# Kernel optimization log

Hardware: AMD Instinct MI355X
Metric: run time of the kernel (lower is better)

## Reference

```python
import jax, jax.numpy as jnp
import numpy as np

B, L, D, H = 2, 8192, 1024, 16
HD = D // H  # head_dim = 64


def setup_inputs() -> dict:
    key = jax.random.key(0)
    ks = jax.random.split(key, 5)
    s = 1.0 / np.sqrt(D)
    return {
        "x": jax.random.normal(ks[0], (B, L, D), dtype=jnp.float32),
        "Wq": jax.random.normal(ks[1], (D, D), dtype=jnp.float32) * s,
        "bq": jnp.zeros((D,), dtype=jnp.float32),
        "Wk": jax.random.normal(ks[2], (D, D), dtype=jnp.float32) * s,
        "bk": jnp.zeros((D,), dtype=jnp.float32),
        "Wv": jax.random.normal(ks[3], (D, D), dtype=jnp.float32) * s,
        "bv": jnp.zeros((D,), dtype=jnp.float32),
        "Wo": jax.random.normal(ks[4], (D, D), dtype=jnp.float32) * s,
        "bo": jnp.zeros((D,), dtype=jnp.float32),
    }


def _rotary(seq_len, dim):
    pos = jnp.arange(seq_len, dtype=jnp.float32)
    freq = 1.0 / (10000.0 ** (jnp.arange(0, dim, 2, dtype=jnp.float32) / dim))
    ang = pos[:, None] * freq[None, :]               # (L, dim/2)
    sin, cos = jnp.sin(ang), jnp.cos(ang)
    # interleave-duplicate: stack((s,s),-1).reshape(L,dim)  (matches torch code)
    sin = jnp.stack((sin, sin), axis=-1).reshape(seq_len, dim)
    cos = jnp.stack((cos, cos), axis=-1).reshape(seq_len, dim)
    return sin, cos


def _rotate_half(t):
    t1, t2 = jnp.split(t, 2, axis=-1)
    return jnp.concatenate([-t2, t1], axis=-1)


def reference(x, Wq, bq, Wk, bk, Wv, bv, Wo, bo):
    b, l, d = x.shape
    q = (x @ Wq + bq).reshape(b, l, H, HD)
    k = (x @ Wk + bk).reshape(b, l, H, HD)
    v = (x @ Wv + bv).reshape(b, l, H, HD)

    sin, cos = _rotary(l, HD)
    sin = sin[None, :, None, :]  # (1, L, 1, HD)
    cos = cos[None, :, None, :]
    q = q * cos + _rotate_half(q) * sin
    k = k * cos + _rotate_half(k) * sin

    # NOTE: faithful to original — heads NOT transposed to (B,H,L,HD),
    # so scores are (B, L, H, H): attention mixes across heads per position.
    scores = jnp.einsum('blhd,bled->blhe', q, k) / jnp.sqrt(jnp.float32(HD))
    w = jax.nn.softmax(scores, axis=-1)              # dropout = identity (eval)
    out = jnp.einsum('blhe,bled->blhd', w, v).reshape(b, l, d)
    return out @ Wo + bo
```

## Files before the change

kernel.cpp:

```cpp
#include <hip/hip_runtime.h>
#include <hip/hip_bf16.h>

typedef __bf16 bf16_t;
typedef __bf16 bf16x8 __attribute__((ext_vector_type(8)));
typedef float f32x4 __attribute__((ext_vector_type(4)));

#define SEQ_L 8192
#define DMODEL 1024
#define NHEAD 16
#define HDIM 64
static constexpr int MROWS = 2 * SEQ_L;

__device__ __forceinline__ void async_cp16(const bf16_t* g, bf16_t* l) {
  __builtin_amdgcn_global_load_lds(
      (__attribute__((address_space(1))) void*)(void*)(g),
      (__attribute__((address_space(3))) void*)(void*)(l), 16, 0, 0);
}
__device__ __forceinline__ void wg_barrier() { __builtin_amdgcn_s_barrier(); }

__global__ __launch_bounds__(256) void f32_to_bf16_k(const float* __restrict__ in,
                                                     bf16_t* __restrict__ out, int n) {
  int i = (blockIdx.x * 256 + threadIdx.x) * 8;
  if (i >= n) return;
  float4 a = *(const float4*)(in + i);
  float4 b = *(const float4*)(in + i + 4);
  bf16x8 o;
  o[0] = (__bf16)a.x; o[1] = (__bf16)a.y; o[2] = (__bf16)a.z; o[3] = (__bf16)a.w;
  o[4] = (__bf16)b.x; o[5] = (__bf16)b.y; o[6] = (__bf16)b.z; o[7] = (__bf16)b.w;
  *(bf16x8*)(out + i) = o;
}

__global__ __launch_bounds__(256) void w_to_bt_k(
    const float* __restrict__ W0, const float* __restrict__ W1,
    const float* __restrict__ W2, const float* __restrict__ W3,
    bf16_t* __restrict__ T0, bf16_t* __restrict__ T1,
    bf16_t* __restrict__ T2, bf16_t* __restrict__ T3) {
  __shared__ float tile[32][33];
  const int z = blockIdx.z;
  const float* W = (z == 0) ? W0 : (z == 1) ? W1 : (z == 2) ? W2 : W3;
  bf16_t* T = (z == 0) ? T0 : (z == 1) ? T1 : (z == 2) ? T2 : T3;
  const int bx = blockIdx.x, by = blockIdx.y;
  const int tx = threadIdx.x, ty = threadIdx.y;
#pragma unroll
  for (int r = 0; r < 4; ++r)
    tile[ty + r * 8][tx] = W[(size_t)(by * 32 + ty + r * 8) * DMODEL + bx * 32 + tx];
  __syncthreads();
#pragma unroll
  for (int r = 0; r < 4; ++r)
    T[(size_t)(bx * 32 + ty + r * 8) * DMODEL + by * 32 + tx] = (bf16_t)tile[tx][ty + r * 8];
}

__global__ __launch_bounds__(256) void rope_tab_k(float2* __restrict__ tab) {
  int i = blockIdx.x * 256 + threadIdx.x;
  int pos = i >> 5, j = i & 31;
  double freq = pow(10000.0, -(double)j / 32.0);
  double ang = (double)pos * freq;
  tab[i] = make_float2((float)cos(ang), (float)sin(ang));
}

template <int MODE>
__global__ __launch_bounds__(256, 4) void gemm128(
    const bf16_t* __restrict__ A, const bf16_t* __restrict__ Bt,
    const float* __restrict__ b0, const float* __restrict__ b1,
    const float* __restrict__ b2, const float2* __restrict__ rope,
    void* __restrict__ O0, void* __restrict__ O1, void* __restrict__ O2) {
  constexpr int K = DMODEL;
  constexpr int KT = K / 64;
  __shared__ bf16_t As_[128 * 64];
  __shared__ bf16_t Bs_[128 * 64];
  const int tid = threadIdx.x;
  const int lane = tid & 63;
  const int wave = tid >> 6;
  const int wm = wave >> 1;
  const int wn = wave & 1;
  const size_t row0 = (size_t)blockIdx.x * 128;
  const int col0 = blockIdx.y * 128;
  const int fr = lane & 15;
  const int fkb = (lane >> 4) * 16;

  const int srow = lane >> 3;
  const int schunk = (lane & 7) ^ (lane >> 3);
  const bf16_t* gA = A + (row0 + wave * 32 + srow) * K + schunk * 8;
  const bf16_t* gB = Bt + ((size_t)col0 + wave * 32 + srow) * K + schunk * 8;
  bf16_t* lA = As_ + wave * 2048 + lane * 8;
  bf16_t* lB = Bs_ + wave * 2048 + lane * 8;

#define STAGE(j)                                           \
  do {                                                     \
    async_cp16(gA + (j)*64, lA);                           \
    async_cp16(gA + 8 * K + (j)*64, lA + 512);             \
    async_cp16(gA + 16 * K + (j)*64, lA + 1024);           \
    async_cp16(gA + 24 * K + (j)*64, lA + 1536);           \
    async_cp16(gB + (j)*64, lB);                           \
    async_cp16(gB + 8 * K + (j)*64, lB + 512);             \
    async_cp16(gB + 16 * K + (j)*64, lB + 1024);           \
    async_cp16(gB + 24 * K + (j)*64, lB + 1536);           \
  } while (0)
#define RD(base, row, kh)                                                    \
  (*(const bf16x8*)((const char*)(base) +                                    \
                    ((((row)*128) + ((kh)*64 + fkb)) ^ (((row)&7) << 4))))
#define VMCNT(n) asm volatile("s_waitcnt vmcnt(" #n ")")
#define LGKM0() asm volatile("s_waitcnt lgkmcnt(0)")
#define SCHED_FENCE() __builtin_amdgcn_sched_barrier(0)

  f32x4 acc[4][4] = {};
  bf16x8 a4[4], b4[4];

  STAGE(0);
  VMCNT(0);
  wg_barrier();
  SCHED_FENCE();

  for (int m = 0; m < KT; ++m) {
#pragma unroll
    for (int f = 0; f < 4; ++f) a4[f] = RD(As_, wm * 64 + f * 16 + fr, 0);
#pragma unroll
    for (int n = 0; n < 4; ++n) b4[n] = RD(Bs_, wn * 64 + n * 16 + fr, 0);
    __builtin_amdgcn_s_setprio(1);
#pragma unroll
    for (int f = 0; f < 4; ++f)
#pragma unroll
      for (int n = 0; n < 4; ++n)
        acc[f][n] = __builtin_amdgcn_mfma_f32_16x16x32_bf16(a4[f], b4[n], acc[f][n], 0, 0, 0);
    __builtin_amdgcn_s_setprio(0);
#pragma unroll
    for (int f = 0; f < 4; ++f) a4[f] = RD(As_, wm * 64 + f * 16 + fr, 1);
#pragma unroll
    for (int n = 0; n < 4; ++n) b4[n] = RD(Bs_, wn * 64 + n * 16 + fr, 1);
    __builtin_amdgcn_s_setprio(1);
#pragma unroll
    for (int f = 0; f < 4; ++f)
#pragma unroll
      for (int n = 0; n < 4; ++n)
        acc[f][n] = __builtin_amdgcn_mfma_f32_16x16x32_bf16(a4[f], b4[n], acc[f][n], 0, 0, 0);
    __builtin_amdgcn_s_setprio(0);
    LGKM0();
    SCHED_FENCE();
    wg_barrier();
    SCHED_FENCE();
    if (m + 1 < KT) STAGE(m + 1);
    VMCNT(0);
    wg_barrier();
    SCHED_FENCE();
  }
#undef STAGE
#undef RD
#undef VMCNT
#undef LGKM0
#undef SCHED_FENCE

  const int lr = (lane >> 4) * 4;
  const int lc = lane & 15;
  const int gcol = col0 + wn * 64;
  int which = 0;
  const float* bias = b0;
  int ocol = gcol;
  if constexpr (MODE == 0) {
    which = gcol >> 10;
    bias = (which == 0) ? b0 : (which == 1) ? b1 : b2;
    ocol = gcol - (which << 10);
  }
  const bool do_rope = (MODE == 0) && (which < 2);
  bf16_t* Cb = nullptr;
  float* Cf = nullptr;
  if constexpr (MODE == 0)
    Cb = (bf16_t*)((which == 0) ? O0 : (which == 1) ? O1 : O2);
  else
    Cf = (float*)O0;

#pragma unroll
  for (int mf = 0; mf < 4; ++mf) {
#pragma unroll
    for (int i = 0; i < 4; ++i) {
      const size_t grow = row0 + wm * 64 + mf * 16 + lr + i;
      float vv[4];
#pragma unroll
      for (int n = 0; n < 4; ++n) vv[n] = acc[mf][n][i] + bias[ocol + n * 16 + lc];
      if (do_rope) {
        const int pos = (int)(grow & (size_t)(SEQ_L - 1));
        const float2* rp = rope + (size_t)pos * 32 + (lc >> 1);
        float rv[4];
#pragma unroll
        for (int n = 0; n < 4; ++n) {
          float2 cs = rp[n * 8];
          rv[n] = (n < 2) ? vv[n] * cs.x - vv[n + 2] * cs.y
                          : vv[n] * cs.x + vv[n - 2] * cs.y;
        }
#pragma unroll
        for (int n = 0; n < 4; ++n) vv[n] = rv[n];
      }
      const size_t cbase = grow * (size_t)DMODEL + ocol + lc;
      if constexpr (MODE == 1) {
#pragma unroll
        for (int n = 0; n < 4; ++n) Cf[cbase + n * 16] = vv[n];
      } else {
#pragma unroll
        for (int n = 0; n < 4; ++n) Cb[cbase + n * 16] = (bf16_t)vv[n];
      }
    }
  }
}

__global__ __launch_bounds__(256) void attn_heads_k(const bf16_t* __restrict__ qb,
                                                    const bf16_t* __restrict__ kb,
                                                    const bf16_t* __restrict__ vb,
                                                    bf16_t* __restrict__ ob) {
  const int t = blockIdx.x * 256 + threadIdx.x;
  const int row = t >> 4;
  const int h = t & 15;
  const size_t rbase = (size_t)row * DMODEL;

  float q[HDIM];
#pragma unroll
  for (int j = 0; j < 8; ++j) {
    bf16x8 v8 = *(const bf16x8*)(qb + rbase + h * HDIM + j * 8);
#pragma unroll
    for (int u = 0; u < 8; ++u) q[j * 8 + u] = (float)v8[u];
  }
  float s[NHEAD];
#pragma unroll
  for (int e = 0; e < NHEAD; ++e) {
    float a = 0.f;
#pragma unroll
    for (int j = 0; j < 8; ++j) {
      bf16x8 k8 = *(const bf16x8*)(kb + rbase + e * HDIM + j * 8);
#pragma unroll
      for (int u = 0; u < 8; ++u) a += q[j * 8 + u] * (float)k8[u];
    }
    s[e] = a * 0.125f;
  }
  float mx = s[0];
#pragma unroll
  for (int e = 1; e < NHEAD; ++e) mx = fmaxf(mx, s[e]);
  float sum = 0.f;
#pragma unroll
  for (int e = 0; e < NHEAD; ++e) {
    s[e] = __expf(s[e] - mx);
    sum += s[e];
  }
  const float inv = 1.f / sum;
  float o[HDIM] = {};
#pragma unroll
  for (int e = 0; e < NHEAD; ++e) {
    const float w = s[e] * inv;
#pragma unroll
    for (int j = 0; j < 8; ++j) {
      bf16x8 v8 = *(const bf16x8*)(vb + rbase + e * HDIM + j * 8);
#pragma unroll
      for (int u = 0; u < 8; ++u) o[j * 8 + u] += w * (float)v8[u];
    }
  }
#pragma unroll
  for (int j = 0; j < 8; ++j) {
    bf16x8 st;
#pragma unroll
    for (int u = 0; u < 8; ++u) st[u] = (__bf16)o[j * 8 + u];
    *(bf16x8*)(ob + rbase + h * HDIM + j * 8) = st;
  }
}

extern "C" void kernel_launch(void* const* d_in, const int* in_sizes, int n_in,
                              void* d_out, int out_size, void* d_ws, size_t ws_size,
                              hipStream_t stream) {
  const float* x = (const float*)d_in[0];
  const float* Wq = (const float*)d_in[1];
  const float* bq = (const float*)d_in[2];
  const float* Wk = (const float*)d_in[3];
  const float* bk = (const float*)d_in[4];
  const float* Wv = (const float*)d_in[5];
  const float* bv = (const float*)d_in[6];
  const float* Wo = (const float*)d_in[7];
  const float* bo = (const float*)d_in[8];

  const int M = MROWS, N = DMODEL, K = DMODEL;

  char* p = (char*)d_ws;
  bf16_t* xb = (bf16_t*)p;    p += (size_t)M * K * 2;
  bf16_t* Wqkvt = (bf16_t*)p; p += (size_t)3 * N * K * 2;
  bf16_t* Wot = (bf16_t*)p;   p += (size_t)N * K * 2;
  bf16_t* qb = (bf16_t*)p;    p += (size_t)M * N * 2;
  bf16_t* kb = (bf16_t*)p;    p += (size_t)M * N * 2;
  bf16_t* vb = (bf16_t*)p;    p += (size_t)M * N * 2;
  bf16_t* ab = (bf16_t*)p;    p += (size_t)M * N * 2;
  float2* rope = (float2*)p;  p += (size_t)SEQ_L * 32 * sizeof(float2);

  bf16_t* Wqt = Wqkvt;
  bf16_t* Wkt = Wqkvt + (size_t)N * K;
  bf16_t* Wvt = Wqkvt + (size_t)2 * N * K;

  f32_to_bf16_k<<<(M * K) / (256 * 8), 256, 0, stream>>>(x, xb, M * K);
  w_to_bt_k<<<dim3(32, 32, 4), dim3(32, 8), 0, stream>>>(Wq, Wk, Wv, Wo, Wqt, Wkt, Wvt, Wot);
  rope_tab_k<<<(SEQ_L * 32) / 256, 256, 0, stream>>>(rope);

  gemm128<0><<<dim3(M / 128, (3 * N) / 128), 256, 0, stream>>>(
      xb, Wqkvt, bq, bk, bv, rope, (void*)qb, (void*)kb, (void*)vb);
  attn_heads_k<<<(M * NHEAD) / 256, 256, 0, stream>>>(qb, kb, vb, ab);
  gemm128<1><<<dim3(M / 128, N / 128), 256, 0, stream>>>(
      ab, Wot, bo, nullptr, nullptr, nullptr, d_out, nullptr, nullptr);
}
```

Measured before the change: 230.5 us.

## Double-buffer GEMM LDS tiles with BK=32 to overlap loads and MFMA

Replaces the single-buffered 64-wide K tile with two 32-wide LDS buffers. The next tile's async global-to-LDS copy is issued before computing on the current buffer, so load latency can overlap MFMA work and one barrier per step is dropped. The XOR swizzle is removed in favour of a plain 32-element row layout, which may add LDS bank conflicts on the fragment reads. There are also twice as many K steps, each with a full vmcnt wait and barrier.

```diff
diff --git a/kernel.cpp b/kernel.cpp
--- a/kernel.cpp
+++ b/kernel.cpp
@@ -65,9 +65,9 @@
     const float* __restrict__ b2, const float2* __restrict__ rope,
     void* __restrict__ O0, void* __restrict__ O1, void* __restrict__ O2) {
   constexpr int K = DMODEL;
-  constexpr int KT = K / 64;
-  __shared__ bf16_t As_[128 * 64];
-  __shared__ bf16_t Bs_[128 * 64];
+  constexpr int NS = K / 32;
+  __shared__ bf16_t As_[2][128 * 32];
+  __shared__ bf16_t Bs_[2][128 * 32];
   const int tid = threadIdx.x;
   const int lane = tid & 63;
   const int wave = tid >> 6;
@@ -76,77 +76,58 @@
   const size_t row0 = (size_t)blockIdx.x * 128;
   const int col0 = blockIdx.y * 128;
   const int fr = lane & 15;
-  const int fkb = (lane >> 4) * 16;
-
-  const int srow = lane >> 3;
-  const int schunk = (lane & 7) ^ (lane >> 3);
-  const bf16_t* gA = A + (row0 + wave * 32 + srow) * K + schunk * 8;
-  const bf16_t* gB = Bt + ((size_t)col0 + wave * 32 + srow) * K + schunk * 8;
-  bf16_t* lA = As_ + wave * 2048 + lane * 8;
-  bf16_t* lB = Bs_ + wave * 2048 + lane * 8;
-
-#define STAGE(j)                                           \
+  const int fke = (lane >> 4) * 8;
+
+  const bf16_t* gA = A + (row0 + (tid >> 2)) * K + (tid & 3) * 8;
+  const bf16_t* gB = Bt + ((size_t)col0 + (tid >> 2)) * K + (tid & 3) * 8;
+
+#define STAGE(j, buf)                                      \
   do {                                                     \
-    async_cp16(gA + (j)*64, lA);                           \
-    async_cp16(gA + 8 * K + (j)*64, lA + 512);             \
-    async_cp16(gA + 16 * K + (j)*64, lA + 1024);           \
-    async_cp16(gA + 24 * K + (j)*64, lA + 1536);           \
-    async_cp16(gB + (j)*64, lB);                           \
-    async_cp16(gB + 8 * K + (j)*64, lB + 512);             \
-    async_cp16(gB + 16 * K + (j)*64, lB + 1024);           \
-    async_cp16(gB + 24 * K + (j)*64, lB + 1536);           \
+    async_cp16(gA + (j)*32, &As_[buf][tid * 8]);           \
+    async_cp16(gA + 64 * K + (j)*32, &As_[buf][2048 + tid * 8]); \
+    async_cp16(gB + (j)*32, &Bs_[buf][tid * 8]);           \
+    async_cp16(gB + 64 * K + (j)*32, &Bs_[buf][2048 + tid * 8]); \
   } while (0)
-#define RD(base, row, kh)                                                    \
-  (*(const bf16x8*)((const char*)(base) +                                    \
-                    ((((row)*128) + ((kh)*64 + fkb)) ^ (((row)&7) << 4))))
+#define RD(base, row) (*(const bf16x8*)((base) + (row)*32 + fke))
 #define VMCNT(n) asm volatile("s_waitcnt vmcnt(" #n ")")
-#define LGKM0() asm volatile("s_waitcnt lgkmcnt(0)")
 #define SCHED_FENCE() __builtin_amdgcn_sched_barrier(0)
 
   f32x4 acc[4][4] = {};
   bf16x8 a4[4], b4[4];
 
-  STAGE(0);
+#define KSTEP(CUR, DO_STAGE, JNEXT)                                            \
+  do {                                                                         \
+    if (DO_STAGE) STAGE(JNEXT, (CUR) ^ 1);                                     \
+    _Pragma("unroll") for (int f = 0; f < 4; ++f)                              \
+        a4[f] = RD(As_[CUR], wm * 64 + f * 16 + fr);                           \
+    _Pragma("unroll") for (int n = 0; n < 4; ++n)                              \
+        b4[n] = RD(Bs_[CUR], wn * 64 + n * 16 + fr);                           \
+    __builtin_amdgcn_s_setprio(1);                                             \
+    _Pragma("unroll") for (int f = 0; f < 4; ++f)                              \
+        _Pragma("unroll") for (int n = 0; n < 4; ++n)                          \
+            acc[f][n] = __builtin_amdgcn_mfma_f32_16x16x32_bf16(               \
+                a4[f], b4[n], acc[f][n], 0, 0, 0);                             \
+    __builtin_amdgcn_s_setprio(0);                                             \
+    VMCNT(0);                                                                  \
+    wg_barrier();                                                              \
+    SCHED_FENCE();                                                             \
+  } while (0)
+
+  STAGE(0, 0);
   VMCNT(0);
   wg_barrier();
   SCHED_FENCE();
 
-  for (int m = 0; m < KT; ++m) {
-#pragma unroll
-    for (int f = 0; f < 4; ++f) a4[f] = RD(As_, wm * 64 + f * 16 + fr, 0);
-#pragma unroll
-    for (int n = 0; n < 4; ++n) b4[n] = RD(Bs_, wn * 64 + n * 16 + fr, 0);
-    __builtin_amdgcn_s_setprio(1);
-#pragma unroll
-    for (int f = 0; f < 4; ++f)
-#pragma unroll
-      for (int n = 0; n < 4; ++n)
-        acc[f][n] = __builtin_amdgcn_mfma_f32_16x16x32_bf16(a4[f], b4[n], acc[f][n], 0, 0, 0);
-    __builtin_amdgcn_s_setprio(0);
-#pragma unroll
-    for (int f = 0; f < 4; ++f) a4[f] = RD(As_, wm * 64 + f * 16 + fr, 1);
-#pragma unroll
-    for (int n = 0; n < 4; ++n) b4[n] = RD(Bs_, wn * 64 + n * 16 + fr, 1);
-    __builtin_amdgcn_s_setprio(1);
-#pragma unroll
-    for (int f = 0; f < 4; ++f)
-#pragma unroll
-      for (int n = 0; n < 4; ++n)
-        acc[f][n] = __builtin_amdgcn_mfma_f32_16x16x32_bf16(a4[f], b4[n], acc[f][n], 0, 0, 0);
-    __builtin_amdgcn_s_setprio(0);
-    LGKM0();
-    SCHED_FENCE();
-    wg_barrier();
-    SCHED_FENCE();
-    if (m + 1 < KT) STAGE(m + 1);
-    VMCNT(0);
-    wg_barrier();
-    SCHED_FENCE();
-  }
+#pragma unroll 1
+  for (int mm = 0; mm < NS / 2; ++mm) {
+    const int m0 = 2 * mm;
+    KSTEP(0, true, m0 + 1);
+    KSTEP(1, (mm < NS / 2 - 1), m0 + 2);
+  }
+#undef KSTEP
 #undef STAGE
 #undef RD
 #undef VMCNT
-#undef LGKM0
 #undef SCHED_FENCE
 
   const int lr = (lane >> 4) * 4;
```

Result: slower. 249.6 us (+8.3%).

## Fuse fp32-to-bf16 input conversion into QKV GEMM A-tile loading

Applied to the files above, without the earlier changes.

Removes the separate kernel that converted x to bf16. The QKV GEMM now async-copies fp32 x tiles into a larger swizzled LDS buffer and converts to bf16 when forming MFMA fragments. This drops a full read/write pass over the activation and a launch. The cost is doubled A-tile global and LDS traffic per GEMM block, extra conversion instructions in the inner loop, and higher LDS use that may reduce occupancy.

```diff
diff --git a/kernel.cpp b/kernel.cpp
--- a/kernel.cpp
+++ b/kernel.cpp
@@ -11,24 +11,12 @@
 #define HDIM 64
 static constexpr int MROWS = 2 * SEQ_L;
 
-__device__ __forceinline__ void async_cp16(const bf16_t* g, bf16_t* l) {
+__device__ __forceinline__ void async_cp16(const void* g, bf16_t* l) {
   __builtin_amdgcn_global_load_lds(
       (__attribute__((address_space(1))) void*)(void*)(g),
       (__attribute__((address_space(3))) void*)(void*)(l), 16, 0, 0);
 }
 __device__ __forceinline__ void wg_barrier() { __builtin_amdgcn_s_barrier(); }
-
-__global__ __launch_bounds__(256) void f32_to_bf16_k(const float* __restrict__ in,
-                                                     bf16_t* __restrict__ out, int n) {
-  int i = (blockIdx.x * 256 + threadIdx.x) * 8;
-  if (i >= n) return;
-  float4 a = *(const float4*)(in + i);
-  float4 b = *(const float4*)(in + i + 4);
-  bf16x8 o;
-  o[0] = (__bf16)a.x; o[1] = (__bf16)a.y; o[2] = (__bf16)a.z; o[3] = (__bf16)a.w;
-  o[4] = (__bf16)b.x; o[5] = (__bf16)b.y; o[6] = (__bf16)b.z; o[7] = (__bf16)b.w;
-  *(bf16x8*)(out + i) = o;
-}
 
 __global__ __launch_bounds__(256) void w_to_bt_k(
     const float* __restrict__ W0, const float* __restrict__ W1,
@@ -60,13 +48,13 @@
 
 template <int MODE>
 __global__ __launch_bounds__(256, 4) void gemm128(
-    const bf16_t* __restrict__ A, const bf16_t* __restrict__ Bt,
+    const void* __restrict__ Araw, const bf16_t* __restrict__ Bt,
     const float* __restrict__ b0, const float* __restrict__ b1,
     const float* __restrict__ b2, const float2* __restrict__ rope,
     void* __restrict__ O0, void* __restrict__ O1, void* __restrict__ O2) {
   constexpr int K = DMODEL;
   constexpr int KT = K / 64;
-  __shared__ bf16_t As_[128 * 64];
+  __shared__ bf16_t As_[(MODE == 0 ? 2 : 1) * 128 * 64];
   __shared__ bf16_t Bs_[128 * 64];
   const int tid = threadIdx.x;
   const int lane = tid & 63;
@@ -76,46 +64,78 @@
   const size_t row0 = (size_t)blockIdx.x * 128;
   const int col0 = blockIdx.y * 128;
   const int fr = lane & 15;
-  const int fkb = (lane >> 4) * 16;
 
   const int srow = lane >> 3;
-  const int schunk = (lane & 7) ^ (lane >> 3);
-  const bf16_t* gA = A + (row0 + wave * 32 + srow) * K + schunk * 8;
+  const int schunk = (lane & 7) ^ srow;
   const bf16_t* gB = Bt + ((size_t)col0 + wave * 32 + srow) * K + schunk * 8;
-  bf16_t* lA = As_ + wave * 2048 + lane * 8;
   bf16_t* lB = Bs_ + wave * 2048 + lane * 8;
 
-#define STAGE(j)                                           \
-  do {                                                     \
-    async_cp16(gA + (j)*64, lA);                           \
-    async_cp16(gA + 8 * K + (j)*64, lA + 512);             \
-    async_cp16(gA + 16 * K + (j)*64, lA + 1024);           \
-    async_cp16(gA + 24 * K + (j)*64, lA + 1536);           \
-    async_cp16(gB + (j)*64, lB);                           \
-    async_cp16(gB + 8 * K + (j)*64, lB + 512);             \
-    async_cp16(gB + 16 * K + (j)*64, lB + 1024);           \
-    async_cp16(gB + 24 * K + (j)*64, lB + 1536);           \
-  } while (0)
-#define RD(base, row, kh)                                                    \
-  (*(const bf16x8*)((const char*)(base) +                                    \
-                    ((((row)*128) + ((kh)*64 + fkb)) ^ (((row)&7) << 4))))
+  const float* gAf = nullptr;
+  const bf16_t* gAb = nullptr;
+  if constexpr (MODE == 0) {
+    const int l16 = (tid & 15) ^ ((tid >> 4) & 7);
+    gAf = (const float*)Araw + (row0 + (tid >> 4)) * (size_t)K + l16 * 4;
+  } else {
+    gAb = (const bf16_t*)Araw + (row0 + wave * 32 + srow) * (size_t)K + schunk * 8;
+  }
+  bf16_t* lA1 = As_ + wave * 2048 + lane * 8;
+
 #define VMCNT(n) asm volatile("s_waitcnt vmcnt(" #n ")")
 #define LGKM0() asm volatile("s_waitcnt lgkmcnt(0)")
 #define SCHED_FENCE() __builtin_amdgcn_sched_barrier(0)
 
+  auto stage = [&](int j) {
+    if constexpr (MODE == 0) {
+#pragma unroll
+      for (int c = 0; c < 8; ++c)
+        async_cp16(gAf + (size_t)c * 16 * K + j * 64, As_ + c * 2048 + tid * 8);
+    } else {
+#pragma unroll
+      for (int c = 0; c < 4; ++c)
+        async_cp16(gAb + (size_t)c * 8 * K + j * 64, lA1 + c * 512);
+    }
+#pragma unroll
+    for (int c = 0; c < 4; ++c)
+      async_cp16(gB + (size_t)c * 8 * K + j * 64, lB + c * 512);
+  };
+
+  auto read_a = [&](int f, int h) -> bf16x8 {
+    const int R = wm * 64 + f * 16 + fr;
+    if constexpr (MODE == 0) {
+      const int c0 = h * 8 + (lane >> 4) * 2;
+      const char* b = (const char*)As_;
+      f32x4 lo = *(const f32x4*)(b + (size_t)R * 256 + (((c0 + 0) ^ (R & 7)) << 4));
+      f32x4 hi = *(const f32x4*)(b + (size_t)R * 256 + (((c0 + 1) ^ (R & 7)) << 4));
+      bf16x8 v;
+      v[0] = (__bf16)lo[0]; v[1] = (__bf16)lo[1]; v[2] = (__bf16)lo[2]; v[3] = (__bf16)lo[3];
+      v[4] = (__bf16)hi[0]; v[5] = (__bf16)hi[1]; v[6] = (__bf16)hi[2]; v[7] = (__bf16)hi[3];
+      return v;
+    } else {
+      const char* b = (const char*)As_;
+      return *(const bf16x8*)(b + (size_t)R * 128 +
+                              (((h * 4 + (lane >> 4)) ^ (R & 7)) << 4));
+    }
+  };
+  auto read_b = [&](int n, int h) -> bf16x8 {
+    const int R = wn * 64 + n * 16 + fr;
+    const char* b = (const char*)Bs_;
+    return *(const bf16x8*)(b + (size_t)R * 128 +
+                            (((h * 4 + (lane >> 4)) ^ (R & 7)) << 4));
+  };
+
   f32x4 acc[4][4] = {};
   bf16x8 a4[4], b4[4];
 
-  STAGE(0);
+  stage(0);
   VMCNT(0);
   wg_barrier();
   SCHED_FENCE();
 
   for (int m = 0; m < KT; ++m) {
 #pragma unroll
-    for (int f = 0; f < 4; ++f) a4[f] = RD(As_, wm * 64 + f * 16 + fr, 0);
-#pragma unroll
-    for (int n = 0; n < 4; ++n) b4[n] = RD(Bs_, wn * 64 + n * 16 + fr, 0);
+    for (int f = 0; f < 4; ++f) a4[f] = read_a(f, 0);
+#pragma unroll
+    for (int n = 0; n < 4; ++n) b4[n] = read_b(n, 0);
     __builtin_amdgcn_s_setprio(1);
 #pragma unroll
     for (int f = 0; f < 4; ++f)
@@ -124,9 +144,9 @@
         acc[f][n] = __builtin_amdgcn_mfma_f32_16x16x32_bf16(a4[f], b4[n], acc[f][n], 0, 0, 0);
     __builtin_amdgcn_s_setprio(0);
 #pragma unroll
-    for (int f = 0; f < 4; ++f) a4[f] = RD(As_, wm * 64 + f * 16 + fr, 1);
-#pragma unroll
-    for (int n = 0; n < 4; ++n) b4[n] = RD(Bs_, wn * 64 + n * 16 + fr, 1);
+    for (int f = 0; f < 4; ++f) a4[f] = read_a(f, 1);
+#pragma unroll
+    for (int n = 0; n < 4; ++n) b4[n] = read_b(n, 1);
     __builtin_amdgcn_s_setprio(1);
 #pragma unroll
     for (int f = 0; f < 4; ++f)
@@ -138,13 +158,11 @@
     SCHED_FENCE();
     wg_barrier();
     SCHED_FENCE();
-    if (m + 1 < KT) STAGE(m + 1);
+    if (m + 1 < KT) stage(m + 1);
     VMCNT(0);
     wg_barrier();
     SCHED_FENCE();
   }
-#undef STAGE
-#undef RD
 #undef VMCNT
 #undef LGKM0
 #undef SCHED_FENCE
@@ -275,7 +293,6 @@
   const int M = MROWS, N = DMODEL, K = DMODEL;
 
   char* p = (char*)d_ws;
-  bf16_t* xb = (bf16_t*)p;    p += (size_t)M * K * 2;
   bf16_t* Wqkvt = (bf16_t*)p; p += (size_t)3 * N * K * 2;
   bf16_t* Wot = (bf16_t*)p;   p += (size_t)N * K * 2;
   bf16_t* qb = (bf16_t*)p;    p += (size_t)M * N * 2;
@@ -288,13 +305,12 @@
   bf16_t* Wkt = Wqkvt + (size_t)N * K;
   bf16_t* Wvt = Wqkvt + (size_t)2 * N * K;
 
-  f32_to_bf16_k<<<(M * K) / (256 * 8), 256, 0, stream>>>(x, xb, M * K);
   w_to_bt_k<<<dim3(32, 32, 4), dim3(32, 8), 0, stream>>>(Wq, Wk, Wv, Wo, Wqt, Wkt, Wvt, Wot);
   rope_tab_k<<<(SEQ_L * 32) / 256, 256, 0, stream>>>(rope);
 
   gemm128<0><<<dim3(M / 128, (3 * N) / 128), 256, 0, stream>>>(
-      xb, Wqkvt, bq, bk, bv, rope, (void*)qb, (void*)kb, (void*)vb);
+      (const void*)x, Wqkvt, bq, bk, bv, rope, (void*)qb, (void*)kb, (void*)vb);
   attn_heads_k<<<(M * NHEAD) / 256, 256, 0, stream>>>(qb, kb, vb, ab);
   gemm128<1><<<dim3(M / 128, N / 128), 256, 0, stream>>>(
-      ab, Wot, bo, nullptr, nullptr, nullptr, d_out, nullptr, nullptr);
-}
+      (const void*)ab, Wot, bo, nullptr, nullptr, nullptr, d_out, nullptr, nullptr);
+}
```

Result: slower. 261.9 us (median of 2 runs) (+13.7%).

## Enlarge GEMM block tile to 256x128 with 8x4 MFMA fragments per wave

Applied to the files above, without the earlier changes.

Both projection GEMMs now use a 256x128 block tile in place of 128x128. Each wave covers 128x64 outputs with a 32-accumulator register tile, and the async LDS staging is rewritten so all 256 threads load rows with an XOR swizzle. This raises arithmetic intensity per LDS/global byte and halves the number of blocks along M. The cost is more registers and LDS per block, with occupancy lowered to 2 blocks per SIMD group, and fewer blocks for the output GEMM (64x8 = 512).

```diff
diff --git a/kernel.cpp b/kernel.cpp
--- a/kernel.cpp
+++ b/kernel.cpp
@@ -11,7 +11,7 @@
 #define HDIM 64
 static constexpr int MROWS = 2 * SEQ_L;
 
-__device__ __forceinline__ void async_cp16(const bf16_t* g, bf16_t* l) {
+__device__ __forceinline__ void async_cp16(const void* g, bf16_t* l) {
   __builtin_amdgcn_global_load_lds(
       (__attribute__((address_space(1))) void*)(void*)(g),
       (__attribute__((address_space(3))) void*)(void*)(l), 16, 0, 0);
@@ -59,97 +59,90 @@
 }
 
 template <int MODE>
-__global__ __launch_bounds__(256, 4) void gemm128(
+__global__ __launch_bounds__(256, 2) void gemm256x128(
     const bf16_t* __restrict__ A, const bf16_t* __restrict__ Bt,
     const float* __restrict__ b0, const float* __restrict__ b1,
     const float* __restrict__ b2, const float2* __restrict__ rope,
     void* __restrict__ O0, void* __restrict__ O1, void* __restrict__ O2) {
   constexpr int K = DMODEL;
   constexpr int KT = K / 64;
-  __shared__ bf16_t As_[128 * 64];
+  __shared__ bf16_t As_[256 * 64];
   __shared__ bf16_t Bs_[128 * 64];
   const int tid = threadIdx.x;
   const int lane = tid & 63;
   const int wave = tid >> 6;
   const int wm = wave >> 1;
   const int wn = wave & 1;
-  const size_t row0 = (size_t)blockIdx.x * 128;
+  const size_t row0 = (size_t)blockIdx.x * 256;
   const int col0 = blockIdx.y * 128;
   const int fr = lane & 15;
-  const int fkb = (lane >> 4) * 16;
-
-  const int srow = lane >> 3;
-  const int schunk = (lane & 7) ^ (lane >> 3);
-  const bf16_t* gA = A + (row0 + wave * 32 + srow) * K + schunk * 8;
-  const bf16_t* gB = Bt + ((size_t)col0 + wave * 32 + srow) * K + schunk * 8;
-  bf16_t* lA = As_ + wave * 2048 + lane * 8;
-  bf16_t* lB = Bs_ + wave * 2048 + lane * 8;
-
-#define STAGE(j)                                           \
-  do {                                                     \
-    async_cp16(gA + (j)*64, lA);                           \
-    async_cp16(gA + 8 * K + (j)*64, lA + 512);             \
-    async_cp16(gA + 16 * K + (j)*64, lA + 1024);           \
-    async_cp16(gA + 24 * K + (j)*64, lA + 1536);           \
-    async_cp16(gB + (j)*64, lB);                           \
-    async_cp16(gB + 8 * K + (j)*64, lB + 512);             \
-    async_cp16(gB + 16 * K + (j)*64, lB + 1024);           \
-    async_cp16(gB + 24 * K + (j)*64, lB + 1536);           \
-  } while (0)
-#define RD(base, row, kh)                                                    \
-  (*(const bf16x8*)((const char*)(base) +                                    \
-                    ((((row)*128) + ((kh)*64 + fkb)) ^ (((row)&7) << 4))))
+  const int g4 = lane >> 4;
+
+  const int srow = tid >> 3;
+  const int sch = (tid & 7) ^ ((tid >> 3) & 7);
+  const bf16_t* gA = A + (row0 + srow) * K + sch * 8;
+  const bf16_t* gB = Bt + ((size_t)col0 + srow) * K + sch * 8;
+
 #define VMCNT(n) asm volatile("s_waitcnt vmcnt(" #n ")")
 #define LGKM0() asm volatile("s_waitcnt lgkmcnt(0)")
 #define SCHED_FENCE() __builtin_amdgcn_sched_barrier(0)
 
-  f32x4 acc[4][4] = {};
-  bf16x8 a4[4], b4[4];
-
-  STAGE(0);
+  auto stage = [&](int j) {
+#pragma unroll
+    for (int c = 0; c < 8; ++c)
+      async_cp16(gA + (size_t)(32 * c) * K + j * 64, As_ + c * 2048 + tid * 8);
+#pragma unroll
+    for (int c = 0; c < 4; ++c)
+      async_cp16(gB + (size_t)(32 * c) * K + j * 64, Bs_ + c * 2048 + tid * 8);
+  };
+  auto read_a = [&](int f, int h) -> bf16x8 {
+    const int R = wm * 128 + f * 16 + fr;
+    return *(const bf16x8*)((const char*)As_ + (size_t)R * 128 +
+                            (((h * 4 + g4) ^ (R & 7)) << 4));
+  };
+  auto read_b = [&](int n, int h) -> bf16x8 {
+    const int R = wn * 64 + n * 16 + fr;
+    return *(const bf16x8*)((const char*)Bs_ + (size_t)R * 128 +
+                            (((h * 4 + g4) ^ (R & 7)) << 4));
+  };
+
+  f32x4 acc[8][4] = {};
+  bf16x8 a8[8], b4[4];
+
+  stage(0);
   VMCNT(0);
   wg_barrier();
   SCHED_FENCE();
 
   for (int m = 0; m < KT; ++m) {
 #pragma unroll
-    for (int f = 0; f < 4; ++f) a4[f] = RD(As_, wm * 64 + f * 16 + fr, 0);
-#pragma unroll
-    for (int n = 0; n < 4; ++n) b4[n] = RD(Bs_, wn * 64 + n * 16 + fr, 0);
-    __builtin_amdgcn_s_setprio(1);
-#pragma unroll
-    for (int f = 0; f < 4; ++f)
-#pragma unroll
-      for (int n = 0; n < 4; ++n)
-        acc[f][n] = __builtin_amdgcn_mfma_f32_16x16x32_bf16(a4[f], b4[n], acc[f][n], 0, 0, 0);
-    __builtin_amdgcn_s_setprio(0);
-#pragma unroll
-    for (int f = 0; f < 4; ++f) a4[f] = RD(As_, wm * 64 + f * 16 + fr, 1);
-#pragma unroll
-    for (int n = 0; n < 4; ++n) b4[n] = RD(Bs_, wn * 64 + n * 16 + fr, 1);
-    __builtin_amdgcn_s_setprio(1);
-#pragma unroll
-    for (int f = 0; f < 4; ++f)
-#pragma unroll
-      for (int n = 0; n < 4; ++n)
-        acc[f][n] = __builtin_amdgcn_mfma_f32_16x16x32_bf16(a4[f], b4[n], acc[f][n], 0, 0, 0);
-    __builtin_amdgcn_s_setprio(0);
+    for (int h = 0; h < 2; ++h) {
+#pragma unroll
+      for (int f = 0; f < 8; ++f) a8[f] = read_a(f, h);
+#pragma unroll
+      for (int n = 0; n < 4; ++n) b4[n] = read_b(n, h);
+      __builtin_amdgcn_s_setprio(1);
+#pragma unroll
+      for (int f = 0; f < 8; ++f)
+#pragma unroll
+        for (int n = 0; n < 4; ++n)
+          acc[f][n] = __builtin_amdgcn_mfma_f32_16x16x32_bf16(a8[f], b4[n], acc[f][n], 0, 0, 0);
+      __builtin_amdgcn_s_setprio(0);
+    }
     LGKM0();
     SCHED_FENCE();
     wg_barrier();
     SCHED_FENCE();
-    if (m + 1 < KT) STAGE(m + 1);
+    if (m + 1 < KT) stage(m + 1);
     VMCNT(0);
     wg_barrier();
     SCHED_FENCE();
   }
-#undef STAGE
-#undef RD
 #undef VMCNT
 #undef LGKM0
 #undef SCHED_FENCE
 
-  const int lr = (lane >> 4) * 4;
+  const int lr = g4 * 4;
   const int lc = lane & 15;
   const int gcol = col0 + wn * 64;
   int which = 0;
@@ -169,10 +162,10 @@
     Cf = (float*)O0;
 
 #pragma unroll
-  for (int mf = 0; mf < 4; ++mf) {
+  for (int mf = 0; mf < 8; ++mf) {
 #pragma unroll
     for (int i = 0; i < 4; ++i) {
-      const size_t grow = row0 + wm * 64 + mf * 16 + lr + i;
+      const size_t grow = row0 + wm * 128 + mf * 16 + lr + i;
       float vv[4];
 #pragma unroll
       for (int n = 0; n < 4; ++n) vv[n] = acc[mf][n][i] + bias[ocol + n * 16 + lc];
@@ -292,9 +285,9 @@
   w_to_bt_k<<<dim3(32, 32, 4), dim3(32, 8), 0, stream>>>(Wq, Wk, Wv, Wo, Wqt, Wkt, Wvt, Wot);
   rope_tab_k<<<(SEQ_L * 32) / 256, 256, 0, stream>>>(rope);
 
-  gemm128<0><<<dim3(M / 128, (3 * N) / 128), 256, 0, stream>>>(
+  gemm256x128<0><<<dim3(M / 256, (3 * N) / 128), 256, 0, stream>>>(
       xb, Wqkvt, bq, bk, bv, rope, (void*)qb, (void*)kb, (void*)vb);
   attn_heads_k<<<(M * NHEAD) / 256, 256, 0, stream>>>(qb, kb, vb, ab);
-  gemm128<1><<<dim3(M / 128, N / 128), 256, 0, stream>>>(
+  gemm256x128<1><<<dim3(M / 256, N / 128), 256, 0, stream>>>(
       ab, Wot, bo, nullptr, nullptr, nullptr, d_out, nullptr, nullptr);
 }
```

New measurement: 225.5 us. 2.1% less time.
